# Optimization experiments

Hardware: AMD Instinct MI355X
Metric: run time of the kernel (lower is better)

The kernel has to match this reference:

```python
import jax, jax.numpy as jnp
from jax import lax
import numpy as np


def _conv2d(x, w, b, pad):
    # x: [N,C,H,W], w: [O,I,kh,kw] (torch OIHW layout)
    y = lax.conv_general_dilated(
        x, w, window_strides=(1, 1), padding=[(pad, pad), (pad, pad)],
        dimension_numbers=("NCHW", "OIHW", "NCHW"))
    return y + b[None, :, None, None]


def _upsample_depth(depth, mask, ratio=2):
    # depth: [N,H,W], mask: [N, 9*ratio*ratio, H, W]
    N, H, W = depth.shape
    m = mask.reshape(N, 9, ratio, ratio, H, W)
    m = jax.nn.softmax(m, axis=1)  # softmax over the 9 taps
    # 3x3 unfold with padding=1, torch F.unfold ordering: (ky, kx) row-major
    padded = jnp.pad(depth, ((0, 0), (1, 1), (1, 1)))
    patches = jnp.stack(
        [padded[:, ky:ky + H, kx:kx + W] for ky in range(3) for kx in range(3)],
        axis=1)  # [N,9,H,W]
    # weighted sum over taps, then interleave: (N,1,a,b,H,W) -> permute(0,1,4,2,5,3)
    up = jnp.einsum("nkabhw,nkhw->nhawb", m, patches)  # [N,H,a,W,b]
    return up.reshape(N, ratio * H, ratio * W)


def setup_inputs() -> dict:
    key = jax.random.key(0)
    ks = jax.random.split(key, 6)
    N, H, W = 4, 512, 640
    in_ch = 8
    depth = jax.random.normal(ks[0], (N, H, W), dtype=jnp.float32)
    cost_volume = jax.random.normal(ks[1], (N, 1, in_ch, H, W), dtype=jnp.float32)
    s1 = 1.0 / np.sqrt(in_ch * 9)
    conv1_w = jax.random.uniform(ks[2], (in_ch, in_ch, 3, 3), jnp.float32, -s1, s1)
    conv1_b = jax.random.uniform(ks[3], (in_ch,), jnp.float32, -s1, s1)
    s2 = 1.0 / np.sqrt(in_ch)
    conv2_w = jax.random.uniform(ks[4], (36, in_ch, 1, 1), jnp.float32, -s2, s2)
    conv2_b = jax.random.uniform(ks[5], (36,), jnp.float32, -s2, s2)
    return {"depth": depth, "cost_volume": cost_volume,
            "conv1_w": conv1_w, "conv1_b": conv1_b,
            "conv2_w": conv2_w, "conv2_b": conv2_b}


def reference(depth, cost_volume, conv1_w, conv1_b, conv2_w, conv2_b):
    b, c, d, h, w = cost_volume.shape
    x = cost_volume.reshape(b, c * d, h, w)
    x = jax.nn.relu(_conv2d(x, conv1_w, conv1_b, pad=1))
    mask = 0.25 * _conv2d(x, conv2_w, conv2_b, pad=0)
    return _upsample_depth(depth, mask, ratio=2)
```

## Files before the change

### kernel.cpp

```cpp
#include <hip/hip_runtime.h>

typedef _Float16 half8  __attribute__((ext_vector_type(8)));
typedef __fp16   fp16x2 __attribute__((ext_vector_type(2)));
typedef float    float4_t __attribute__((ext_vector_type(4)));

#define SH 4
#define SW 160
#define CW (SW + 2)
#define NR (SH + 2)
#define DW (CW + 1)

template <int CTRL>
__device__ __forceinline__ float rr_add(float v) {
    const int i = __float_as_int(v);
    const int p = __builtin_amdgcn_update_dpp(i, i, CTRL, 0xF, 0xF, false);
    return v + __int_as_float(p);
}
#define ROR4 0x124
#define ROR8 0x128

__global__ __launch_bounds__(256, 4) void depth_up_fused(
    const float* __restrict__ depth,
    const float* __restrict__ cv,
    const float* __restrict__ w1,
    const float* __restrict__ b1,
    const float* __restrict__ w2,
    const float* __restrict__ b2,
    float* __restrict__ out)
{
    const int H = 512, W = 640;
    const size_t HW = (size_t)H * W;
    const int n  = blockIdx.z;
    const int h0 = blockIdx.y * SH;
    const int cb = blockIdx.x * SW;
    const int tid  = threadIdx.x;
    const int lane = tid & 63;
    const int wv   = tid >> 6;
    const int o    = lane & 15;
    const int krow = lane >> 4;
    const int u    = o >> 2;
    const int q    = o & 3;

    __shared__ half8 s_cv[NR * CW];
    __shared__ float s_d[NR * DW];

    const float* __restrict__ cvn = cv + (size_t)n * 8 * HW;
    const float* __restrict__ dn  = depth + (size_t)n * HW;

    #pragma unroll
    for (int j = 0; j < 4; ++j) {
        const int i0 = tid + 256 * j;
        const int it = i0 < (NR * CW - 1) ? i0 : (NR * CW - 1);
        const int r  = it / CW;
        const int c  = it - r * CW;
        const int gh = h0 + r - 1;
        const int gw = cb + c - 1;
        const int ghs = gh < 0 ? 0 : (gh > H - 1 ? H - 1 : gh);
        const int gws = gw < 0 ? 0 : (gw > W - 1 ? W - 1 : gw);
        const bool ok = (gh == ghs) & (gw == gws);
        const float* p = cvn + (size_t)ghs * W + gws;
        float f[9];
        #pragma unroll
        for (int ch = 0; ch < 8; ++ch) f[ch] = p[(size_t)ch * HW];
        f[8] = dn[(size_t)ghs * W + gws];
        #pragma unroll
        for (int k = 0; k < 9; ++k) f[k] = ok ? f[k] : 0.0f;
        union { half8 v8; fp16x2 h2[4]; } hu;
        #pragma unroll
        for (int pq = 0; pq < 4; ++pq)
            hu.h2[pq] = __builtin_amdgcn_cvt_pkrtz(f[2 * pq], f[2 * pq + 1]);
        s_cv[r * CW + c] = hu.v8;
        s_d[r * DW + c]  = f[8];
    }

    half8 a1[3];
    #pragma unroll
    for (int ki = 0; ki < 3; ++ki) {
        const int tap = 4 * ki + krow;
        #pragma unroll
        for (int j = 0; j < 8; ++j)
            a1[ki][j] = (tap < 9 && o < 8) ? (_Float16)w1[(o * 8 + j) * 9 + tap]
                                           : (_Float16)0.0f;
    }
    int aoff[3];
    #pragma unroll
    for (int ki = 0; ki < 3; ++ki) {
        const int tap0 = 4 * ki + krow;
        const int tap  = tap0 > 8 ? 8 : tap0;
        const int ky   = tap / 3;
        const int kx   = tap - 3 * ky;
        aoff[ki] = ((wv + ky) * CW + o + kx) * 16;
    }
    const float4_t b1q = *reinterpret_cast<const float4_t*>(b1 + (krow & 1) * 4);

    half8 b2f[3] = {};
    if (krow == 0) {
        #pragma unroll
        for (int t = 0; t < 3; ++t) {
            const int m = (o + 16 * t) > 35 ? 35 : (o + 16 * t);
            const float4_t wlo = *reinterpret_cast<const float4_t*>(w2 + m * 8);
            const float4_t whi = *reinterpret_cast<const float4_t*>(w2 + m * 8 + 4);
            #pragma unroll
            for (int j = 0; j < 4; ++j) {
                b2f[t][j]     = (_Float16)wlo[j];
                b2f[t][4 + j] = (_Float16)whi[j];
            }
        }
    }
    const float C = 0.25f * 1.44269504f;
    float b2q[3];
    #pragma unroll
    for (int t = 0; t < 3; ++t) {
        const int m = (o + 16 * t) > 35 ? 35 : (o + 16 * t);
        b2q[t] = C * b2[m];
    }
    if (u != 0) b2q[2] = -1.0e38f;

    int poff[3];
    {
        const int taps[3] = {u, u + 4, 8};
        #pragma unroll
        for (int t = 0; t < 3; ++t) {
            const int ky = taps[t] / 3;
            const int kx = taps[t] - 3 * ky;
            poff[t] = ((wv + ky) * DW + kx) * 4;
        }
    }

    __syncthreads();

    const char* cvb = (const char*)s_cv;
    const char* sdb = (const char*)s_d;
    const float4_t zero4 = {0.0f, 0.0f, 0.0f, 0.0f};

    const half8* bb0 = (const half8*)(cvb + aoff[0]);
    const half8* bb1 = (const half8*)(cvb + aoff[1]);
    const half8* bb2 = (const half8*)(cvb + aoff[2]);
    const float* pb0 = (const float*)(sdb + poff[0] + krow * 16);
    const float* pb1 = (const float*)(sdb + poff[1] + krow * 16);
    const float* pb2 = (const float*)(sdb + poff[2] + krow * 16);
    float* ob = out + ((size_t)n * 1024 + (size_t)(2 * (h0 + wv) + (q >> 1))) * 1280
                    + (size_t)(2 * (cb + 4 * krow + u) + (q & 1));

    auto body = [&](int ps) __attribute__((always_inline)) -> float {
        const half8 c0 = bb0[ps * 16];
        const half8 c1 = bb1[ps * 16];
        const half8 c2 = bb2[ps * 16];

        float4_t acc1 = zero4;
        acc1 = __builtin_amdgcn_mfma_f32_16x16x32_f16(a1[0], c0, acc1, 0, 0, 0);
        acc1 = __builtin_amdgcn_mfma_f32_16x16x32_f16(a1[1], c1, acc1, 0, 0, 0);
        acc1 = __builtin_amdgcn_mfma_f32_16x16x32_f16(a1[2], c2, acc1, 0, 0, 0);

        union { half8 v; fp16x2 h2[4]; uint32_t u32[4]; } a2;
        const float x0 = fmaxf(acc1[0] + b1q[0], 0.0f);
        const float x1 = fmaxf(acc1[1] + b1q[1], 0.0f);
        const float x2 = fmaxf(acc1[2] + b1q[2], 0.0f);
        const float x3 = fmaxf(acc1[3] + b1q[3], 0.0f);
        a2.h2[0] = __builtin_amdgcn_cvt_pkrtz(x0, x1);
        a2.h2[1] = __builtin_amdgcn_cvt_pkrtz(x2, x3);
        a2.u32[2] = (uint32_t)__shfl_xor((int)a2.u32[0], 16);
        a2.u32[3] = (uint32_t)__shfl_xor((int)a2.u32[1], 16);

        const float4_t d2_0 = __builtin_amdgcn_mfma_f32_16x16x32_f16(a2.v, b2f[0], zero4, 0, 0, 0);
        const float4_t d2_1 = __builtin_amdgcn_mfma_f32_16x16x32_f16(a2.v, b2f[1], zero4, 0, 0, 0);
        const float4_t d2_2 = __builtin_amdgcn_mfma_f32_16x16x32_f16(a2.v, b2f[2], zero4, 0, 0, 0);

        float se[4], sp[4];
        #pragma unroll
        for (int r = 0; r < 4; ++r) {
            const float e0 = __builtin_amdgcn_exp2f(fmaf(d2_0[r], C, b2q[0]));
            const float e1 = __builtin_amdgcn_exp2f(fmaf(d2_1[r], C, b2q[1]));
            const float e2 = __builtin_amdgcn_exp2f(fmaf(d2_2[r], C, b2q[2]));
            const float pt0 = pb0[ps * 16 + r];
            const float pt1 = pb1[ps * 16 + r];
            const float pt2 = pb2[ps * 16 + r];
            se[r] = e0 + e1 + e2;
            sp[r] = e0 * pt0 + e1 * pt1 + e2 * pt2;
        }
        #pragma unroll
        for (int r = 0; r < 4; ++r) {
            se[r] = rr_add<ROR8>(rr_add<ROR4>(se[r]));
            sp[r] = rr_add<ROR8>(rr_add<ROR4>(sp[r]));
        }
        float res[4];
        #pragma unroll
        for (int r = 0; r < 4; ++r) res[r] = sp[r] * __builtin_amdgcn_rcpf(se[r]);
        const float v01 = (u & 1) ? res[1] : res[0];
        const float v23 = (u & 1) ? res[3] : res[2];
        return (u & 2) ? v23 : v01;
    };

    for (int pp = 0; pp < 5; ++pp) {
        const float vA = body(pp);
        const float vB = body(pp + 5);
        ob[pp * 32]       = vA;
        ob[(pp + 5) * 32] = vB;
    }
}

extern "C" void kernel_launch(void* const* d_in, const int* in_sizes, int n_in,
                              void* d_out, int out_size, void* d_ws, size_t ws_size,
                              hipStream_t stream) {
    (void)in_sizes; (void)n_in; (void)out_size; (void)d_ws; (void)ws_size;
    const float* depth = (const float*)d_in[0];
    const float* cv    = (const float*)d_in[1];
    const float* w1    = (const float*)d_in[2];
    const float* b1    = (const float*)d_in[3];
    const float* w2    = (const float*)d_in[4];
    const float* b2    = (const float*)d_in[5];
    float* out = (float*)d_out;

    dim3 grid(640 / SW, 512 / SH, 4);
    dim3 block(256);
    hipLaunchKernelGGL(depth_up_fused, grid, block, 0, stream,
                       depth, cv, w1, b1, w2, b2, out);
}
```

Baseline: 44.81 us.

## Split conv1 MFMA into two half-channel passes and software-pipeline LDS loads

Conv1 now runs as two MFMA chains, each producing four output channels, so the conv2 A operand can be assembled in registers without the two cross-lane shuffles. The main loop is also software-pipelined: shared-memory operands and depth taps for the next pixel group are loaded while the current group computes. This doubles conv1 MFMA issue and raises register pressure under the 4-wave launch bound, in exchange for removing the shuffles and hiding LDS latency.

Measured after the change: 48.02 us. +7.2%, slower.

```diff
diff --git a/kernel.cpp b/kernel.cpp
--- a/kernel.cpp
+++ b/kernel.cpp
@@ -73,14 +73,17 @@
         s_d[r * DW + c]  = f[8];
     }
 
-    half8 a1[3];
+    half8 a1a[3], a1b[3];
     #pragma unroll
     for (int ki = 0; ki < 3; ++ki) {
         const int tap = 4 * ki + krow;
         #pragma unroll
-        for (int j = 0; j < 8; ++j)
-            a1[ki][j] = (tap < 9 && o < 8) ? (_Float16)w1[(o * 8 + j) * 9 + tap]
-                                           : (_Float16)0.0f;
+        for (int j = 0; j < 8; ++j) {
+            a1a[ki][j] = (tap < 9 && o < 4) ? (_Float16)w1[(o * 8 + j) * 9 + tap]
+                                            : (_Float16)0.0f;
+            a1b[ki][j] = (tap < 9 && o < 4) ? (_Float16)w1[((o + 4) * 8 + j) * 9 + tap]
+                                            : (_Float16)0.0f;
+        }
     }
     int aoff[3];
     #pragma unroll
@@ -91,7 +94,8 @@
         const int kx   = tap - 3 * ky;
         aoff[ki] = ((wv + ky) * CW + o + kx) * 16;
     }
-    const float4_t b1q = *reinterpret_cast<const float4_t*>(b1 + (krow & 1) * 4);
+    const float4_t b1a = *reinterpret_cast<const float4_t*>(b1);
+    const float4_t b1b = *reinterpret_cast<const float4_t*>(b1 + 4);
 
     half8 b2f[3] = {};
     if (krow == 0) {
@@ -142,25 +146,42 @@
     float* ob = out + ((size_t)n * 1024 + (size_t)(2 * (h0 + wv) + (q >> 1))) * 1280
                     + (size_t)(2 * (cb + 4 * krow + u) + (q & 1));
 
-    auto body = [&](int ps) __attribute__((always_inline)) -> float {
-        const half8 c0 = bb0[ps * 16];
-        const half8 c1 = bb1[ps * 16];
-        const half8 c2 = bb2[ps * 16];
-
-        float4_t acc1 = zero4;
-        acc1 = __builtin_amdgcn_mfma_f32_16x16x32_f16(a1[0], c0, acc1, 0, 0, 0);
-        acc1 = __builtin_amdgcn_mfma_f32_16x16x32_f16(a1[1], c1, acc1, 0, 0, 0);
-        acc1 = __builtin_amdgcn_mfma_f32_16x16x32_f16(a1[2], c2, acc1, 0, 0, 0);
-
-        union { half8 v; fp16x2 h2[4]; uint32_t u32[4]; } a2;
-        const float x0 = fmaxf(acc1[0] + b1q[0], 0.0f);
-        const float x1 = fmaxf(acc1[1] + b1q[1], 0.0f);
-        const float x2 = fmaxf(acc1[2] + b1q[2], 0.0f);
-        const float x3 = fmaxf(acc1[3] + b1q[3], 0.0f);
-        a2.h2[0] = __builtin_amdgcn_cvt_pkrtz(x0, x1);
-        a2.h2[1] = __builtin_amdgcn_cvt_pkrtz(x2, x3);
-        a2.u32[2] = (uint32_t)__shfl_xor((int)a2.u32[0], 16);
-        a2.u32[3] = (uint32_t)__shfl_xor((int)a2.u32[1], 16);
+    half8 c0 = bb0[0], c1 = bb1[0], c2 = bb2[0];
+    float pt0[4], pt1[4], pt2[4];
+    #pragma unroll
+    for (int r = 0; r < 4; ++r) {
+        pt0[r] = pb0[r]; pt1[r] = pb1[r]; pt2[r] = pb2[r];
+    }
+
+    #pragma unroll 2
+    for (int pp = 0; pp < SW / 16; ++pp) {
+        const int np = (pp + 1 < SW / 16) ? pp + 1 : pp;
+        half8 nc0 = bb0[np * 16], nc1 = bb1[np * 16], nc2 = bb2[np * 16];
+        float n0[4], n1[4], n2[4];
+        #pragma unroll
+        for (int r = 0; r < 4; ++r) {
+            n0[r] = pb0[np * 16 + r];
+            n1[r] = pb1[np * 16 + r];
+            n2[r] = pb2[np * 16 + r];
+        }
+
+        float4_t accA = zero4, accB = zero4;
+        accA = __builtin_amdgcn_mfma_f32_16x16x32_f16(a1a[0], c0, accA, 0, 0, 0);
+        accB = __builtin_amdgcn_mfma_f32_16x16x32_f16(a1b[0], c0, accB, 0, 0, 0);
+        accA = __builtin_amdgcn_mfma_f32_16x16x32_f16(a1a[1], c1, accA, 0, 0, 0);
+        accB = __builtin_amdgcn_mfma_f32_16x16x32_f16(a1b[1], c1, accB, 0, 0, 0);
+        accA = __builtin_amdgcn_mfma_f32_16x16x32_f16(a1a[2], c2, accA, 0, 0, 0);
+        accB = __builtin_amdgcn_mfma_f32_16x16x32_f16(a1b[2], c2, accB, 0, 0, 0);
+
+        union { half8 v; fp16x2 h2[4]; } a2;
+        a2.h2[0] = __builtin_amdgcn_cvt_pkrtz(fmaxf(accA[0] + b1a[0], 0.0f),
+                                              fmaxf(accA[1] + b1a[1], 0.0f));
+        a2.h2[1] = __builtin_amdgcn_cvt_pkrtz(fmaxf(accA[2] + b1a[2], 0.0f),
+                                              fmaxf(accA[3] + b1a[3], 0.0f));
+        a2.h2[2] = __builtin_amdgcn_cvt_pkrtz(fmaxf(accB[0] + b1b[0], 0.0f),
+                                              fmaxf(accB[1] + b1b[1], 0.0f));
+        a2.h2[3] = __builtin_amdgcn_cvt_pkrtz(fmaxf(accB[2] + b1b[2], 0.0f),
+                                              fmaxf(accB[3] + b1b[3], 0.0f));
 
         const float4_t d2_0 = __builtin_amdgcn_mfma_f32_16x16x32_f16(a2.v, b2f[0], zero4, 0, 0, 0);
         const float4_t d2_1 = __builtin_amdgcn_mfma_f32_16x16x32_f16(a2.v, b2f[1], zero4, 0, 0, 0);
@@ -172,30 +193,29 @@
             const float e0 = __builtin_amdgcn_exp2f(fmaf(d2_0[r], C, b2q[0]));
             const float e1 = __builtin_amdgcn_exp2f(fmaf(d2_1[r], C, b2q[1]));
             const float e2 = __builtin_amdgcn_exp2f(fmaf(d2_2[r], C, b2q[2]));
-            const float pt0 = pb0[ps * 16 + r];
-            const float pt1 = pb1[ps * 16 + r];
-            const float pt2 = pb2[ps * 16 + r];
             se[r] = e0 + e1 + e2;
-            sp[r] = e0 * pt0 + e1 * pt1 + e2 * pt2;
+            sp[r] = e0 * pt0[r] + e1 * pt1[r] + e2 * pt2[r];
         }
         #pragma unroll
         for (int r = 0; r < 4; ++r) {
             se[r] = rr_add<ROR8>(rr_add<ROR4>(se[r]));
             sp[r] = rr_add<ROR8>(rr_add<ROR4>(sp[r]));
         }
+
         float res[4];
         #pragma unroll
         for (int r = 0; r < 4; ++r) res[r] = sp[r] * __builtin_amdgcn_rcpf(se[r]);
+
         const float v01 = (u & 1) ? res[1] : res[0];
         const float v23 = (u & 1) ? res[3] : res[2];
-        return (u & 2) ? v23 : v01;
-    };
-
-    for (int pp = 0; pp < 5; ++pp) {
-        const float vA = body(pp);
-        const float vB = body(pp + 5);
-        ob[pp * 32]       = vA;
-        ob[(pp + 5) * 32] = vB;
+        const float val = (u & 2) ? v23 : v01;
+        ob[pp * 32] = val;
+
+        c0 = nc0; c1 = nc1; c2 = nc2;
+        #pragma unroll
+        for (int r = 0; r < 4; ++r) {
+            pt0[r] = n0[r]; pt1[r] = n1[r]; pt2[r] = n2[r];
+        }
     }
 }
 
```

## Split into padded fp16 pack pass plus global-read compute kernel

Applied to the files above, without the earlier changes.

Adds a pre-pass that converts the 8-channel cost volume into a zero-padded interleaved fp16 half8 array and a padded depth array in workspace. The main kernel then reads MFMA operands straight from global/L2 without staging them in LDS, keeping only depth in shared memory, and raises the occupancy hint. This removes per-block halo and bounds handling and the LDS footprint, but adds a second launch and an extra full write and read of the packed tensors. The old fused kernel is kept as a fallback when the workspace is too small.

New measurement: 54.13 us. 1.21x slower.

```diff
diff --git a/kernel.cpp b/kernel.cpp
--- a/kernel.cpp
+++ b/kernel.cpp
@@ -7,8 +7,10 @@
 #define SH 4
 #define SW 160
 #define CW (SW + 2)
-#define NR (SH + 2)
+#define NR 6
 #define DW (CW + 1)
+#define PH 514
+#define PW 642
 
 template <int CTRL>
 __device__ __forceinline__ float rr_add(float v) {
@@ -19,7 +21,181 @@
 #define ROR4 0x124
 #define ROR8 0x128
 
-__global__ __launch_bounds__(256, 4) void depth_up_fused(
+__global__ __launch_bounds__(256) void pack_tiles(
+    const float* __restrict__ depth,
+    const float* __restrict__ cv,
+    half8* __restrict__ tcv,
+    float* __restrict__ pd)
+{
+    const int H = 512, W = 640;
+    const size_t HW = (size_t)H * W;
+    const int idx = blockIdx.x * 256 + threadIdx.x;
+    const int total = 4 * PH * PW;
+    if (idx >= total) return;
+    const int n   = idx / (PH * PW);
+    const int rem = idx - n * (PH * PW);
+    const int hp  = rem / PW;
+    const int wp  = rem - hp * PW;
+    const int h = hp - 1, w = wp - 1;
+    half8 hv = {};
+    float dv = 0.0f;
+    if ((unsigned)h < (unsigned)H && (unsigned)w < (unsigned)W) {
+        const float* p = cv + (size_t)n * 8 * HW + (size_t)h * W + w;
+        union { half8 v8; fp16x2 h2[4]; } hu;
+        float f[8];
+        #pragma unroll
+        for (int ch = 0; ch < 8; ++ch) f[ch] = p[(size_t)ch * HW];
+        #pragma unroll
+        for (int pq = 0; pq < 4; ++pq)
+            hu.h2[pq] = __builtin_amdgcn_cvt_pkrtz(f[2 * pq], f[2 * pq + 1]);
+        hv = hu.v8;
+        dv = depth[(size_t)n * HW + (size_t)h * W + w];
+    }
+    tcv[idx] = hv;
+    pd[idx]  = dv;
+}
+
+__global__ __launch_bounds__(256, 6) void depth_up_main(
+    const half8* __restrict__ tcv,
+    const float* __restrict__ pd,
+    const float* __restrict__ w1,
+    const float* __restrict__ b1,
+    const float* __restrict__ w2,
+    const float* __restrict__ b2,
+    float* __restrict__ out)
+{
+    const int n  = blockIdx.z;
+    const int h0 = blockIdx.y * SH;
+    const int cb = blockIdx.x * SW;
+    const int tid  = threadIdx.x;
+    const int lane = tid & 63;
+    const int wv   = tid >> 6;
+    const int o    = lane & 15;
+    const int krow = lane >> 4;
+    const int u    = o >> 2;
+    const int q    = o & 3;
+
+    __shared__ float s_d[NR * DW];
+
+    const float* pdn = pd + (size_t)n * PH * PW;
+    for (int i = tid; i < NR * CW; i += 256) {
+        const int r = i / CW;
+        const int c = i - r * CW;
+        s_d[r * DW + c] = pdn[(size_t)(h0 + r) * PW + (cb + c)];
+    }
+
+    half8 a1[3];
+    #pragma unroll
+    for (int ki = 0; ki < 3; ++ki) {
+        const int tap = 4 * ki + krow;
+        #pragma unroll
+        for (int j = 0; j < 8; ++j)
+            a1[ki][j] = (tap < 9 && o < 8) ? (_Float16)w1[(o * 8 + j) * 9 + tap]
+                                           : (_Float16)0.0f;
+    }
+    const half8* tb[3];
+    #pragma unroll
+    for (int ki = 0; ki < 3; ++ki) {
+        const int tap0 = 4 * ki + krow;
+        const int tap  = tap0 > 8 ? 8 : tap0;
+        const int ky   = tap / 3;
+        const int kx   = tap - 3 * ky;
+        tb[ki] = tcv + ((size_t)n * PH + (size_t)(h0 + wv + ky)) * PW + (cb + o + kx);
+    }
+    const float4_t b1q = *reinterpret_cast<const float4_t*>(b1 + (krow & 1) * 4);
+
+    half8 b2f[3] = {};
+    if (krow == 0) {
+        #pragma unroll
+        for (int t = 0; t < 3; ++t) {
+            const int m = (o + 16 * t) > 35 ? 35 : (o + 16 * t);
+            const float4_t wlo = *reinterpret_cast<const float4_t*>(w2 + m * 8);
+            const float4_t whi = *reinterpret_cast<const float4_t*>(w2 + m * 8 + 4);
+            #pragma unroll
+            for (int j = 0; j < 4; ++j) {
+                b2f[t][j]     = (_Float16)wlo[j];
+                b2f[t][4 + j] = (_Float16)whi[j];
+            }
+        }
+    }
+    const float C = 0.25f * 1.44269504f;
+    float b2q[3];
+    #pragma unroll
+    for (int t = 0; t < 3; ++t) {
+        const int m = (o + 16 * t) > 35 ? 35 : (o + 16 * t);
+        b2q[t] = C * b2[m];
+    }
+    if (u != 0) b2q[2] = -1.0e38f;
+
+    int poff[3];
+    {
+        const int taps[3] = {u, u + 4, 8};
+        #pragma unroll
+        for (int t = 0; t < 3; ++t) {
+            const int ky = taps[t] / 3;
+            const int kx = taps[t] - 3 * ky;
+            poff[t] = ((wv + ky) * DW + kx) * 4;
+        }
+    }
+
+    __syncthreads();
+
+    const char* sdb = (const char*)s_d;
+    const float4_t zero4 = {0.0f, 0.0f, 0.0f, 0.0f};
+    const float* pb0 = (const float*)(sdb + poff[0] + krow * 16);
+    const float* pb1 = (const float*)(sdb + poff[1] + krow * 16);
+    const float* pb2 = (const float*)(sdb + poff[2] + krow * 16);
+    float* ob = out + ((size_t)n * 1024 + (size_t)(2 * (h0 + wv) + (q >> 1))) * 1280
+                    + (size_t)(2 * (cb + 4 * krow + u) + (q & 1));
+
+    #pragma unroll 2
+    for (int pp = 0; pp < SW / 16; ++pp) {
+        const half8 c0 = tb[0][pp * 16];
+        const half8 c1 = tb[1][pp * 16];
+        const half8 c2 = tb[2][pp * 16];
+
+        float4_t acc1 = zero4;
+        acc1 = __builtin_amdgcn_mfma_f32_16x16x32_f16(a1[0], c0, acc1, 0, 0, 0);
+        acc1 = __builtin_amdgcn_mfma_f32_16x16x32_f16(a1[1], c1, acc1, 0, 0, 0);
+        acc1 = __builtin_amdgcn_mfma_f32_16x16x32_f16(a1[2], c2, acc1, 0, 0, 0);
+
+        union { half8 v; fp16x2 h2[4]; uint32_t u32[4]; } a2;
+        a2.h2[0] = __builtin_amdgcn_cvt_pkrtz(fmaxf(acc1[0] + b1q[0], 0.0f),
+                                              fmaxf(acc1[1] + b1q[1], 0.0f));
+        a2.h2[1] = __builtin_amdgcn_cvt_pkrtz(fmaxf(acc1[2] + b1q[2], 0.0f),
+                                              fmaxf(acc1[3] + b1q[3], 0.0f));
+        a2.u32[2] = (uint32_t)__shfl_xor((int)a2.u32[0], 16);
+        a2.u32[3] = (uint32_t)__shfl_xor((int)a2.u32[1], 16);
+
+        const float4_t d2_0 = __builtin_amdgcn_mfma_f32_16x16x32_f16(a2.v, b2f[0], zero4, 0, 0, 0);
+        const float4_t d2_1 = __builtin_amdgcn_mfma_f32_16x16x32_f16(a2.v, b2f[1], zero4, 0, 0, 0);
+        const float4_t d2_2 = __builtin_amdgcn_mfma_f32_16x16x32_f16(a2.v, b2f[2], zero4, 0, 0, 0);
+
+        float se[4], sp[4];
+        #pragma unroll
+        for (int r = 0; r < 4; ++r) {
+            const float e0 = __builtin_amdgcn_exp2f(fmaf(d2_0[r], C, b2q[0]));
+            const float e1 = __builtin_amdgcn_exp2f(fmaf(d2_1[r], C, b2q[1]));
+            const float e2 = __builtin_amdgcn_exp2f(fmaf(d2_2[r], C, b2q[2]));
+            se[r] = e0 + e1 + e2;
+            sp[r] = e0 * pb0[pp * 16 + r] + e1 * pb1[pp * 16 + r]
+                  + e2 * pb2[pp * 16 + r];
+        }
+        #pragma unroll
+        for (int r = 0; r < 4; ++r) {
+            se[r] = rr_add<ROR8>(rr_add<ROR4>(se[r]));
+            sp[r] = rr_add<ROR8>(rr_add<ROR4>(sp[r]));
+        }
+        float res[4];
+        #pragma unroll
+        for (int r = 0; r < 4; ++r) res[r] = sp[r] * __builtin_amdgcn_rcpf(se[r]);
+        const float v01 = (u & 1) ? res[1] : res[0];
+        const float v23 = (u & 1) ? res[3] : res[2];
+        ob[pp * 32] = (u & 2) ? v23 : v01;
+    }
+}
+
+__global__ __launch_bounds__(256, 4) void depth_up_fallback(
     const float* __restrict__ depth,
     const float* __restrict__ cv,
     const float* __restrict__ w1,
@@ -142,10 +318,11 @@
     float* ob = out + ((size_t)n * 1024 + (size_t)(2 * (h0 + wv) + (q >> 1))) * 1280
                     + (size_t)(2 * (cb + 4 * krow + u) + (q & 1));
 
-    auto body = [&](int ps) __attribute__((always_inline)) -> float {
-        const half8 c0 = bb0[ps * 16];
-        const half8 c1 = bb1[ps * 16];
-        const half8 c2 = bb2[ps * 16];
+    #pragma unroll 2
+    for (int pp = 0; pp < SW / 16; ++pp) {
+        const half8 c0 = bb0[pp * 16];
+        const half8 c1 = bb1[pp * 16];
+        const half8 c2 = bb2[pp * 16];
 
         float4_t acc1 = zero4;
         acc1 = __builtin_amdgcn_mfma_f32_16x16x32_f16(a1[0], c0, acc1, 0, 0, 0);
@@ -153,12 +330,10 @@
         acc1 = __builtin_amdgcn_mfma_f32_16x16x32_f16(a1[2], c2, acc1, 0, 0, 0);
 
         union { half8 v; fp16x2 h2[4]; uint32_t u32[4]; } a2;
-        const float x0 = fmaxf(acc1[0] + b1q[0], 0.0f);
-        const float x1 = fmaxf(acc1[1] + b1q[1], 0.0f);
-        const float x2 = fmaxf(acc1[2] + b1q[2], 0.0f);
-        const float x3 = fmaxf(acc1[3] + b1q[3], 0.0f);
-        a2.h2[0] = __builtin_amdgcn_cvt_pkrtz(x0, x1);
-        a2.h2[1] = __builtin_amdgcn_cvt_pkrtz(x2, x3);
+        a2.h2[0] = __builtin_amdgcn_cvt_pkrtz(fmaxf(acc1[0] + b1q[0], 0.0f),
+                                              fmaxf(acc1[1] + b1q[1], 0.0f));
+        a2.h2[1] = __builtin_amdgcn_cvt_pkrtz(fmaxf(acc1[2] + b1q[2], 0.0f),
+                                              fmaxf(acc1[3] + b1q[3], 0.0f));
         a2.u32[2] = (uint32_t)__shfl_xor((int)a2.u32[0], 16);
         a2.u32[3] = (uint32_t)__shfl_xor((int)a2.u32[1], 16);
 
@@ -172,11 +347,9 @@
             const float e0 = __builtin_amdgcn_exp2f(fmaf(d2_0[r], C, b2q[0]));
             const float e1 = __builtin_amdgcn_exp2f(fmaf(d2_1[r], C, b2q[1]));
             const float e2 = __builtin_amdgcn_exp2f(fmaf(d2_2[r], C, b2q[2]));
-            const float pt0 = pb0[ps * 16 + r];
-            const float pt1 = pb1[ps * 16 + r];
-            const float pt2 = pb2[ps * 16 + r];
             se[r] = e0 + e1 + e2;
-            sp[r] = e0 * pt0 + e1 * pt1 + e2 * pt2;
+            sp[r] = e0 * pb0[pp * 16 + r] + e1 * pb1[pp * 16 + r]
+                  + e2 * pb2[pp * 16 + r];
         }
         #pragma unroll
         for (int r = 0; r < 4; ++r) {
@@ -188,21 +361,14 @@
         for (int r = 0; r < 4; ++r) res[r] = sp[r] * __builtin_amdgcn_rcpf(se[r]);
         const float v01 = (u & 1) ? res[1] : res[0];
         const float v23 = (u & 1) ? res[3] : res[2];
-        return (u & 2) ? v23 : v01;
-    };
-
-    for (int pp = 0; pp < 5; ++pp) {
-        const float vA = body(pp);
-        const float vB = body(pp + 5);
-        ob[pp * 32]       = vA;
-        ob[(pp + 5) * 32] = vB;
+        ob[pp * 32] = (u & 2) ? v23 : v01;
     }
 }
 
 extern "C" void kernel_launch(void* const* d_in, const int* in_sizes, int n_in,
                               void* d_out, int out_size, void* d_ws, size_t ws_size,
                               hipStream_t stream) {
-    (void)in_sizes; (void)n_in; (void)out_size; (void)d_ws; (void)ws_size;
+    (void)in_sizes; (void)n_in; (void)out_size;
     const float* depth = (const float*)d_in[0];
     const float* cv    = (const float*)d_in[1];
     const float* w1    = (const float*)d_in[2];
@@ -211,8 +377,21 @@
     const float* b2    = (const float*)d_in[5];
     float* out = (float*)d_out;
 
-    dim3 grid(640 / SW, 512 / SH, 4);
-    dim3 block(256);
-    hipLaunchKernelGGL(depth_up_fused, grid, block, 0, stream,
-                       depth, cv, w1, b1, w2, b2, out);
-}
+    const size_t tcv_bytes = (size_t)4 * PH * PW * sizeof(half8);
+    const size_t pd_bytes  = (size_t)4 * PH * PW * sizeof(float);
+
+    if (ws_size >= tcv_bytes + pd_bytes) {
+        half8* tcv = (half8*)d_ws;
+        float* pd  = (float*)((char*)d_ws + tcv_bytes);
+        const int total = 4 * PH * PW;
+        hipLaunchKernelGGL(pack_tiles, dim3((total + 255) / 256), dim3(256), 0, stream,
+                           depth, cv, tcv, pd);
+        dim3 grid(640 / SW, 512 / SH, 4);
+        hipLaunchKernelGGL(depth_up_main, grid, dim3(256), 0, stream,
+                           tcv, pd, w1, b1, w2, b2, out);
+    } else {
+        dim3 grid(640 / SW, 512 / SH, 4);
+        hipLaunchKernelGGL(depth_up_fallback, grid, dim3(256), 0, stream,
+                           depth, cv, w1, b1, w2, b2, out);
+    }
+}
```
